# Performance work log

Hardware: AMD Instinct MI355X
Metric: run time of the kernel (lower is better)

Reference implementation:

```python
import jax, jax.numpy as jnp
import numpy as np

E = 1024
H = 16
HD = E // H


def setup_inputs() -> dict:
    key = jax.random.key(0)
    k1, k2, k3, k4, k5 = jax.random.split(key, 5)
    x = jax.random.normal(k1, (2, 2048, E), dtype=jnp.float32)
    s = 1.0 / np.sqrt(E)
    qkv_w = jax.random.uniform(k2, (3 * E, E), jnp.float32, -s, s)
    qkv_b = jax.random.uniform(k3, (3 * E,), jnp.float32, -s, s)
    o_w = jax.random.uniform(k4, (E, E), jnp.float32, -s, s)
    o_b = jax.random.uniform(k5, (E,), jnp.float32, -s, s)
    return {"x": x, "qkv_w": qkv_w, "qkv_b": qkv_b, "o_w": o_w, "o_b": o_b}


def reference(x, qkv_w, qkv_b, o_w, o_b):
    B, T, _ = x.shape
    # qkv projection (torch Linear: x @ W.T + b)
    qkv = x @ qkv_w.T + qkv_b  # [B,T,3E]
    q, k, v = jnp.split(qkv, 3, axis=-1)
    # [B,H,T,HD]
    q = q.reshape(B, T, H, HD).transpose(0, 2, 1, 3)
    k = k.reshape(B, T, H, HD).transpose(0, 2, 1, 3)
    v = v.reshape(B, T, H, HD).transpose(0, 2, 1, 3)
    scores = jnp.einsum('bhqd,bhkd->bhqk', q, k) / np.sqrt(HD)
    causal = jnp.tril(jnp.ones((T, T), dtype=bool))
    scores = jnp.where(causal, scores, -jnp.inf)
    attn = jax.nn.softmax(scores, axis=-1)  # dropout disabled (eval mode)
    y = jnp.einsum('bhqk,bhkd->bhqd', attn, v)
    y = y.transpose(0, 2, 1, 3).reshape(B, T, E)
    return y @ o_w.T + o_b
```

## Files before the change

kernel.cpp:

```cpp
#include <hip/hip_runtime.h>
#include <hip/hip_bf16.h>
#include <math.h>

#define BATCH 2
#define SEQ   2048
#define EMB   1024
#define NH    16
#define HD    64
#define M_ROWS (BATCH * SEQ)

typedef __attribute__((ext_vector_type(8))) short bf16x8;
typedef __attribute__((ext_vector_type(4))) float f32x4;

__device__ __forceinline__ ushort f2bf(float f) {
    unsigned u = __float_as_uint(f);
    unsigned lsb = (u >> 16) & 1u;
    u += 0x7fffu + lsb;
    return (ushort)(u >> 16);
}

__device__ __forceinline__ unsigned cvt_pk_bf16(float lo, float hi) {
    unsigned r;
    asm("v_cvt_pk_bf16_f32 %0, %1, %2" : "=v"(r) : "v"(lo), "v"(hi));
    return r;
}

__device__ __forceinline__ void gload_lds16(const void* g, void* l) {
    __builtin_amdgcn_global_load_lds(
        (const __attribute__((address_space(1))) unsigned int*)g,
        (__attribute__((address_space(3))) unsigned int*)l, 16, 0, 0);
}

__global__ __launch_bounds__(256) void cvt3_f32_bf16(
    const float* __restrict__ s1, const float* __restrict__ s2,
    const float* __restrict__ s3, ushort* __restrict__ out,
    int n1, int n2)
{
    int i = (blockIdx.x * 256 + threadIdx.x) * 4;
    const float* src;
    int off;
    if (i < n1)            { src = s1; off = i; }
    else if (i < n1 + n2)  { src = s2; off = i - n1; }
    else                   { src = s3; off = i - n1 - n2; }
    float4 v = *reinterpret_cast<const float4*>(&src[off]);
    uint2 pk;
    pk.x = cvt_pk_bf16(v.x, v.y);
    pk.y = cvt_pk_bf16(v.z, v.w);
    *reinterpret_cast<uint2*>(&out[i]) = pk;
}

template <int MODE>
__global__ __launch_bounds__(256) void gemm_mfma_abt(
    const ushort* __restrict__ A, const ushort* __restrict__ B,
    const float* __restrict__ bias, float* __restrict__ Cout,
    ushort* __restrict__ qkb, ushort* __restrict__ vtb,
    int M, int N, int K)
{
    __shared__ ushort Al[128 * 64];
    __shared__ ushort Bl[128 * 64];

    const int tid  = threadIdx.x;
    const int lane = tid & 63;
    const int wave = tid >> 6;
    const int wr   = wave >> 1;
    const int wc   = wave & 1;
    const int l15  = lane & 15;
    const int l4   = lane >> 4;
    const int m0   = blockIdx.y * 128;
    const int n0   = blockIdx.x * 128;

    f32x4 acc[4][4];
#pragma unroll
    for (int m = 0; m < 4; ++m)
#pragma unroll
        for (int n = 0; n < 4; ++n)
#pragma unroll
            for (int r = 0; r < 4; ++r) acc[m][n][r] = 0.f;

    for (int k0 = 0; k0 < K; k0 += 64) {
#pragma unroll
        for (int it = 0; it < 4; ++it) {
            int chunk = tid + it * 256;
            int row = chunk >> 3;
            int kc  = (chunk & 7) * 8;
            gload_lds16(&A[(size_t)(m0 + row) * K + k0 + kc], &Al[chunk * 8]);
            gload_lds16(&B[(size_t)(n0 + row) * K + k0 + kc], &Bl[chunk * 8]);
        }
        __syncthreads();

#pragma unroll
        for (int kk = 0; kk < 2; ++kk) {
            const int ko = kk * 32 + l4 * 8;
            bf16x8 a[4], b[4];
#pragma unroll
            for (int m = 0; m < 4; ++m)
                a[m] = *reinterpret_cast<const bf16x8*>(
                    &Al[(wr * 64 + m * 16 + l15) * 64 + ko]);
#pragma unroll
            for (int n = 0; n < 4; ++n)
                b[n] = *reinterpret_cast<const bf16x8*>(
                    &Bl[(wc * 64 + n * 16 + l15) * 64 + ko]);
            __builtin_amdgcn_s_setprio(1);
#pragma unroll
            for (int m = 0; m < 4; ++m)
#pragma unroll
                for (int n = 0; n < 4; ++n)
                    acc[m][n] = __builtin_amdgcn_mfma_f32_16x16x32_bf16(
                        a[m], b[n], acc[m][n], 0, 0, 0);
            __builtin_amdgcn_s_setprio(0);
        }
        __syncthreads();
    }

#pragma unroll
    for (int n = 0; n < 4; ++n) {
        const int col = n0 + wc * 64 + n * 16 + l15;
        const float bv = bias[col];
        if (MODE == 0) {
#pragma unroll
            for (int m = 0; m < 4; ++m) {
                const int row0 = m0 + wr * 64 + m * 16 + l4 * 4;
#pragma unroll
                for (int r = 0; r < 4; ++r)
                    Cout[(size_t)(row0 + r) * N + col] = acc[m][n][r] + bv;
            }
        } else if (col < 2 * EMB) {
#pragma unroll
            for (int m = 0; m < 4; ++m) {
                const int row0 = m0 + wr * 64 + m * 16 + l4 * 4;
#pragma unroll
                for (int r = 0; r < 4; ++r)
                    qkb[(size_t)(row0 + r) * 2048 + col] = f2bf(acc[m][n][r] + bv);
            }
        } else {
            const int h = (col - 2 * EMB) >> 6;
            const int d = col & 63;
#pragma unroll
            for (int m = 0; m < 4; ++m) {
                const int row0 = m0 + wr * 64 + m * 16 + l4 * 4;
                const int bb = row0 >> 11;
                const int t  = row0 & 2047;
                uint2 pk;
                pk.x = cvt_pk_bf16(acc[m][n][0] + bv, acc[m][n][1] + bv);
                pk.y = cvt_pk_bf16(acc[m][n][2] + bv, acc[m][n][3] + bv);
                *reinterpret_cast<uint2*>(
                    &vtb[((size_t)(bb * 16 + h) * 64 + d) * 2048 + t]) = pk;
            }
        }
    }
}

__global__ __launch_bounds__(512) void attn_mfma(
    const ushort* __restrict__ qk, const ushort* __restrict__ vt,
    ushort* __restrict__ y)
{
    __shared__ alignas(16) ushort Kl[4][4096];
    __shared__ alignas(16) ushort Vl[4][4096];
    __shared__ alignas(16) ushort QP[8192];

    const int tid  = threadIdx.x;
    const int lane = tid & 63;
    const int w    = tid >> 6;
    const int l15  = lane & 15;
    const int l4   = lane >> 4;

    const int id  = blockIdx.x;
    const int xcd = id & 7;
    const int bh  = xcd * 4 + ((id >> 3) & 3);
    const int pp  = id >> 5;
    const int b   = bh >> 4;
    const int h   = bh & 15;

    const ushort* qbase = qk + (size_t)b * SEQ * 2048 + h * HD;
    const ushort* kbase = qbase + EMB;
    const ushort* vbase = vt + (size_t)bh * HD * SEQ;

    const int swz   = (l15 & 7) << 4;
    const int koff0 = ((l4 * 16) ^ swz) >> 1;
    const int koff1 = ((64 + l4 * 16) ^ swz) >> 1;

    int pso[4];
#pragma unroll
    for (int n = 0; n < 4; ++n) pso[n] = ((n * 32 + l4 * 8) ^ swz) >> 1;

    const short OBF = (short)0x3F80;
    const bf16x8 ones = {OBF, OBF, OBF, OBF, OBF, OBF, OBF, OBF};
    const float BETA = 0.18033688f;

    const int qrow = (w * 16 + l15) * 64;

    const int sr = tid >> 3;
    const int sc = ((tid & 7) ^ (sr & 7)) << 3;
    const int i2 = tid + 512;
    const int qr2 = i2 >> 3;
    const int qc2 = ((i2 & 7) ^ (qr2 & 7)) << 3;

#pragma unroll
    for (int pass = 0; pass < 2; ++pass) {
        const int qt  = pass ? (15 - pp) : pp;
        const int nkv = 2 * qt + 2;

        gload_lds16(qbase + (size_t)(qt * 128 + sr) * 2048 + sc, &QP[tid * 8]);
        gload_lds16(qbase + (size_t)(qt * 128 + qr2) * 2048 + qc2, &QP[i2 * 8]);
        gload_lds16(kbase + (size_t)sr * 2048 + sc, &Kl[0][tid * 8]);
        gload_lds16(kbase + (size_t)(64 + sr) * 2048 + sc, &Kl[1][tid * 8]);
        gload_lds16(vbase + (size_t)sr * 2048 + sc, &Vl[0][tid * 8]);
        gload_lds16(vbase + (size_t)sr * 2048 + 64 + sc, &Vl[1][tid * 8]);
        __syncthreads();

        const bf16x8 qf0 = *reinterpret_cast<const bf16x8*>(&QP[qrow + koff0]);
        const bf16x8 qf1 = *reinterpret_cast<const bf16x8*>(&QP[qrow + koff1]);

        f32x4 o[4];
#pragma unroll
        for (int n = 0; n < 4; ++n)
#pragma unroll
            for (int r = 0; r < 4; ++r) o[n][r] = 0.f;
        f32x4 lacc = {0.f, 0.f, 0.f, 0.f};
        float m = -3.0e38f;

        auto computeTile = [&](const ushort* Kb, const ushort* Vb, int kkt) {
            bf16x8 kf[4][2];
#pragma unroll
            for (int n = 0; n < 4; ++n) {
                kf[n][0] = *reinterpret_cast<const bf16x8*>(
                    &Kb[(n * 16 + l15) * 64 + koff0]);
                kf[n][1] = *reinterpret_cast<const bf16x8*>(
                    &Kb[(n * 16 + l15) * 64 + koff1]);
            }
            f32x4 s[4];
            __builtin_amdgcn_s_setprio(1);
#pragma unroll
            for (int n = 0; n < 4; ++n) {
                f32x4 z = {0.f, 0.f, 0.f, 0.f};
                z = __builtin_amdgcn_mfma_f32_16x16x32_bf16(kf[n][0], qf0, z, 0, 0, 0);
                s[n] = __builtin_amdgcn_mfma_f32_16x16x32_bf16(kf[n][1], qf1, z, 0, 0, 0);
            }
            __builtin_amdgcn_s_setprio(0);

            bf16x8 vf[4][2];
#pragma unroll
            for (int n = 0; n < 4; ++n) {
                vf[n][0] = *reinterpret_cast<const bf16x8*>(
                    &Vb[(n * 16 + l15) * 64 + koff0]);
                vf[n][1] = *reinterpret_cast<const bf16x8*>(
                    &Vb[(n * 16 + l15) * 64 + koff1]);
            }

            if (kkt >= nkv - 2) {
                const int q0 = qt * 128 + w * 16 + l15;
#pragma unroll
                for (int n = 0; n < 4; ++n)
#pragma unroll
                    for (int r = 0; r < 4; ++r) {
                        int kg = kkt * 64 + n * 16 + l4 * 4 + r;
                        if (kg > q0) s[n][r] = -3.0e38f;
                    }
            }

            float a0 = fmaxf(fmaxf(s[0][0], s[0][1]), fmaxf(s[0][2], s[0][3]));
            float a1 = fmaxf(fmaxf(s[1][0], s[1][1]), fmaxf(s[1][2], s[1][3]));
            float a2 = fmaxf(fmaxf(s[2][0], s[2][1]), fmaxf(s[2][2], s[2][3]));
            float a3 = fmaxf(fmaxf(s[3][0], s[3][1]), fmaxf(s[3][2], s[3][3]));
            float pm = fmaxf(fmaxf(a0, a1), fmaxf(a2, a3)) * BETA;

            if (__any(pm > m + 8.0f)) {
                float tm = fmaxf(pm, __shfl_xor(pm, 16));
                tm = fmaxf(tm, __shfl_xor(tm, 32));
                float mn = fmaxf(m, tm);
                float al = exp2f(m - mn);
                m = mn;
                float b0 = __shfl(al, l4 * 4 + 0, 16);
                float b1 = __shfl(al, l4 * 4 + 1, 16);
                float b2 = __shfl(al, l4 * 4 + 2, 16);
                float b3 = __shfl(al, l4 * 4 + 3, 16);
                lacc[0] *= b0; lacc[1] *= b1; lacc[2] *= b2; lacc[3] *= b3;
#pragma unroll
                for (int n = 0; n < 4; ++n) {
                    o[n][0] *= b0; o[n][1] *= b1; o[n][2] *= b2; o[n][3] *= b3;
                }
            }

#pragma unroll
            for (int n = 0; n < 4; ++n) {
                float pa = exp2f(fmaf(s[n][0], BETA, -m));
                float pb = exp2f(fmaf(s[n][1], BETA, -m));
                float pc = exp2f(fmaf(s[n][2], BETA, -m));
                float pd = exp2f(fmaf(s[n][3], BETA, -m));
                uint2 pk;
                pk.x = cvt_pk_bf16(pa, pb);
                pk.y = cvt_pk_bf16(pc, pd);
                *reinterpret_cast<uint2*>(&QP[qrow + pso[n]]) = pk;
            }

            bf16x8 pf0 = *reinterpret_cast<const bf16x8*>(&QP[qrow + koff0]);
            bf16x8 pf1 = *reinterpret_cast<const bf16x8*>(&QP[qrow + koff1]);
            __builtin_amdgcn_s_setprio(1);
            lacc = __builtin_amdgcn_mfma_f32_16x16x32_bf16(pf0, ones, lacc, 0, 0, 0);
            lacc = __builtin_amdgcn_mfma_f32_16x16x32_bf16(pf1, ones, lacc, 0, 0, 0);
#pragma unroll
            for (int n = 0; n < 4; ++n) {
                o[n] = __builtin_amdgcn_mfma_f32_16x16x32_bf16(pf0, vf[n][0], o[n], 0, 0, 0);
                o[n] = __builtin_amdgcn_mfma_f32_16x16x32_bf16(pf1, vf[n][1], o[n], 0, 0, 0);
            }
            __builtin_amdgcn_s_setprio(0);
        };

        for (int kk = 0; kk < nkv; kk += 2) {
            if (kk + 2 < nkv) {
                const int b2 = (kk + 2) & 3;
                const int b3 = (kk + 3) & 3;
                gload_lds16(kbase + (size_t)((kk + 2) * 64 + sr) * 2048 + sc,
                            &Kl[b2][tid * 8]);
                gload_lds16(kbase + (size_t)((kk + 3) * 64 + sr) * 2048 + sc,
                            &Kl[b3][tid * 8]);
                gload_lds16(vbase + (size_t)sr * 2048 + (kk + 2) * 64 + sc,
                            &Vl[b2][tid * 8]);
                gload_lds16(vbase + (size_t)sr * 2048 + (kk + 3) * 64 + sc,
                            &Vl[b3][tid * 8]);
            }
            computeTile(Kl[kk & 3], Vl[kk & 3], kk);
            computeTile(Kl[(kk + 1) & 3], Vl[(kk + 1) & 3], kk + 1);
            __syncthreads();
        }

#pragma unroll
        for (int r = 0; r < 4; ++r) {
            float inv = 1.f / lacc[r];
            int row = qt * 128 + w * 16 + l4 * 4 + r;
#pragma unroll
            for (int n = 0; n < 4; ++n) {
                y[(size_t)(b * SEQ + row) * EMB + h * HD + n * 16 + l15] =
                    f2bf(o[n][r] * inv);
            }
        }
        __syncthreads();
    }
}

extern "C" void kernel_launch(void* const* d_in, const int* in_sizes, int n_in,
                              void* d_out, int out_size, void* d_ws, size_t ws_size,
                              hipStream_t stream)
{
    const float* x     = (const float*)d_in[0];
    const float* qkv_w = (const float*)d_in[1];
    const float* qkv_b = (const float*)d_in[2];
    const float* o_w   = (const float*)d_in[3];
    const float* o_b   = (const float*)d_in[4];
    float* out = (float*)d_out;

    ushort* xb    = (ushort*)d_ws;
    ushort* wqkvb = xb    + (size_t)M_ROWS * EMB;
    ushort* owb   = wqkvb + (size_t)3 * EMB * EMB;
    ushort* qkb   = owb   + (size_t)EMB * EMB;
    ushort* vtb   = qkb   + (size_t)M_ROWS * 2 * EMB;
    ushort* ybb   = vtb   + (size_t)32 * HD * SEQ;

    {
        int n1 = M_ROWS * EMB;
        int n2 = 3 * EMB * EMB;
        int ntot = n1 + n2 + EMB * EMB;
        cvt3_f32_bf16<<<ntot / 1024, 256, 0, stream>>>(
            x, qkv_w, o_w, xb, n1, n2);
    }

    {
        dim3 grid(3 * EMB / 128, M_ROWS / 128);
        gemm_mfma_abt<1><<<grid, 256, 0, stream>>>(
            xb, wqkvb, qkv_b, nullptr, qkb, vtb, M_ROWS, 3 * EMB, EMB);
    }

    {
        attn_mfma<<<256, 512, 0, stream>>>(qkb, vtb, ybb);
    }

    {
        dim3 grid(EMB / 128, M_ROWS / 128);
        gemm_mfma_abt<0><<<grid, 256, 0, stream>>>(
            ybb, owb, o_b, out, nullptr, nullptr, M_ROWS, EMB, EMB);
    }
}
```

Before: 113.7 us.

## Split attention KV loop across two wave groups with split-K merge for balanced work

The attention block grows from 512 to 1024 threads. Instead of running the two paired query tiles one after the other, group B handles the first 17 KV tiles of the long query tile. Group A handles its short tile and then the remaining KV tiles of the long tile. The partial softmax states (o, l, m) are merged through LDS at the end. This cuts the serial KV loop per block from 34 tiles to 17 and raises occupancy, at the cost of double-buffered KV loads, an extra LDS merge and more register pressure at the higher launch bound.

```diff
diff --git a/kernel.cpp b/kernel.cpp
--- a/kernel.cpp
+++ b/kernel.cpp
@@ -150,17 +150,18 @@
     }
 }
 
-__global__ __launch_bounds__(512) void attn_mfma(
+__global__ __launch_bounds__(1024) void attn_mfma(
     const ushort* __restrict__ qk, const ushort* __restrict__ vt,
     ushort* __restrict__ y)
 {
-    __shared__ alignas(16) ushort Kl[4][4096];
-    __shared__ alignas(16) ushort Vl[4][4096];
-    __shared__ alignas(16) ushort QP[8192];
+    __shared__ alignas(16) ushort KV[8][4096];
+    __shared__ alignas(16) ushort QP[16384];
 
     const int tid  = threadIdx.x;
     const int lane = tid & 63;
     const int w    = tid >> 6;
+    const int u    = w & 7;
+    const bool isA = (w < 8);
     const int l15  = lane & 15;
     const int l4   = lane >> 4;
 
@@ -168,6 +169,9 @@
     const int xcd = id & 7;
     const int bh  = xcd * 4 + ((id >> 3) & 3);
     const int pp  = id >> 5;
+    const int qtA = pp, qtB = 15 - pp;
+    const int nkvA = 2 * pp + 2;
+    const int nkvB = 32 - 2 * pp;
     const int b   = bh >> 4;
     const int h   = bh & 15;
 
@@ -178,7 +182,6 @@
     const int swz   = (l15 & 7) << 4;
     const int koff0 = ((l4 * 16) ^ swz) >> 1;
     const int koff1 = ((64 + l4 * 16) ^ swz) >> 1;
-
     int pso[4];
 #pragma unroll
     for (int n = 0; n < 4; ++n) pso[n] = ((n * 32 + l4 * 8) ^ swz) >> 1;
@@ -189,152 +192,214 @@
 
     const int qrow = (w * 16 + l15) * 64;
 
-    const int sr = tid >> 3;
-    const int sc = ((tid & 7) ^ (sr & 7)) << 3;
-    const int i2 = tid + 512;
-    const int qr2 = i2 >> 3;
-    const int qc2 = ((i2 & 7) ^ (qr2 & 7)) << 3;
-
-#pragma unroll
-    for (int pass = 0; pass < 2; ++pass) {
-        const int qt  = pass ? (15 - pp) : pp;
-        const int nkv = 2 * qt + 2;
-
-        gload_lds16(qbase + (size_t)(qt * 128 + sr) * 2048 + sc, &QP[tid * 8]);
-        gload_lds16(qbase + (size_t)(qt * 128 + qr2) * 2048 + qc2, &QP[i2 * 8]);
-        gload_lds16(kbase + (size_t)sr * 2048 + sc, &Kl[0][tid * 8]);
-        gload_lds16(kbase + (size_t)(64 + sr) * 2048 + sc, &Kl[1][tid * 8]);
-        gload_lds16(vbase + (size_t)sr * 2048 + sc, &Vl[0][tid * 8]);
-        gload_lds16(vbase + (size_t)sr * 2048 + 64 + sc, &Vl[1][tid * 8]);
-        __syncthreads();
-
-        const bf16x8 qf0 = *reinterpret_cast<const bf16x8*>(&QP[qrow + koff0]);
-        const bf16x8 qf1 = *reinterpret_cast<const bf16x8*>(&QP[qrow + koff1]);
-
-        f32x4 o[4];
-#pragma unroll
-        for (int n = 0; n < 4; ++n)
-#pragma unroll
-            for (int r = 0; r < 4; ++r) o[n][r] = 0.f;
-        f32x4 lacc = {0.f, 0.f, 0.f, 0.f};
-        float m = -3.0e38f;
-
-        auto computeTile = [&](const ushort* Kb, const ushort* Vb, int kkt) {
-            bf16x8 kf[4][2];
-#pragma unroll
-            for (int n = 0; n < 4; ++n) {
-                kf[n][0] = *reinterpret_cast<const bf16x8*>(
-                    &Kb[(n * 16 + l15) * 64 + koff0]);
-                kf[n][1] = *reinterpret_cast<const bf16x8*>(
-                    &Kb[(n * 16 + l15) * 64 + koff1]);
-            }
-            f32x4 s[4];
-            __builtin_amdgcn_s_setprio(1);
-#pragma unroll
-            for (int n = 0; n < 4; ++n) {
-                f32x4 z = {0.f, 0.f, 0.f, 0.f};
-                z = __builtin_amdgcn_mfma_f32_16x16x32_bf16(kf[n][0], qf0, z, 0, 0, 0);
-                s[n] = __builtin_amdgcn_mfma_f32_16x16x32_bf16(kf[n][1], qf1, z, 0, 0, 0);
-            }
-            __builtin_amdgcn_s_setprio(0);
-
-            bf16x8 vf[4][2];
-#pragma unroll
-            for (int n = 0; n < 4; ++n) {
-                vf[n][0] = *reinterpret_cast<const bf16x8*>(
-                    &Vb[(n * 16 + l15) * 64 + koff0]);
-                vf[n][1] = *reinterpret_cast<const bf16x8*>(
-                    &Vb[(n * 16 + l15) * 64 + koff1]);
-            }
-
-            if (kkt >= nkv - 2) {
-                const int q0 = qt * 128 + w * 16 + l15;
-#pragma unroll
-                for (int n = 0; n < 4; ++n)
-#pragma unroll
-                    for (int r = 0; r < 4; ++r) {
-                        int kg = kkt * 64 + n * 16 + l4 * 4 + r;
-                        if (kg > q0) s[n][r] = -3.0e38f;
-                    }
-            }
-
-            float a0 = fmaxf(fmaxf(s[0][0], s[0][1]), fmaxf(s[0][2], s[0][3]));
-            float a1 = fmaxf(fmaxf(s[1][0], s[1][1]), fmaxf(s[1][2], s[1][3]));
-            float a2 = fmaxf(fmaxf(s[2][0], s[2][1]), fmaxf(s[2][2], s[2][3]));
-            float a3 = fmaxf(fmaxf(s[3][0], s[3][1]), fmaxf(s[3][2], s[3][3]));
-            float pm = fmaxf(fmaxf(a0, a1), fmaxf(a2, a3)) * BETA;
-
-            if (__any(pm > m + 8.0f)) {
-                float tm = fmaxf(pm, __shfl_xor(pm, 16));
-                tm = fmaxf(tm, __shfl_xor(tm, 32));
-                float mn = fmaxf(m, tm);
-                float al = exp2f(m - mn);
-                m = mn;
-                float b0 = __shfl(al, l4 * 4 + 0, 16);
-                float b1 = __shfl(al, l4 * 4 + 1, 16);
-                float b2 = __shfl(al, l4 * 4 + 2, 16);
-                float b3 = __shfl(al, l4 * 4 + 3, 16);
-                lacc[0] *= b0; lacc[1] *= b1; lacc[2] *= b2; lacc[3] *= b3;
-#pragma unroll
-                for (int n = 0; n < 4; ++n) {
-                    o[n][0] *= b0; o[n][1] *= b1; o[n][2] *= b2; o[n][3] *= b3;
-                }
-            }
-
-#pragma unroll
-            for (int n = 0; n < 4; ++n) {
-                float pa = exp2f(fmaf(s[n][0], BETA, -m));
-                float pb = exp2f(fmaf(s[n][1], BETA, -m));
-                float pc = exp2f(fmaf(s[n][2], BETA, -m));
-                float pd = exp2f(fmaf(s[n][3], BETA, -m));
-                uint2 pk;
-                pk.x = cvt_pk_bf16(pa, pb);
-                pk.y = cvt_pk_bf16(pc, pd);
-                *reinterpret_cast<uint2*>(&QP[qrow + pso[n]]) = pk;
-            }
-
-            bf16x8 pf0 = *reinterpret_cast<const bf16x8*>(&QP[qrow + koff0]);
-            bf16x8 pf1 = *reinterpret_cast<const bf16x8*>(&QP[qrow + koff1]);
-            __builtin_amdgcn_s_setprio(1);
-            lacc = __builtin_amdgcn_mfma_f32_16x16x32_bf16(pf0, ones, lacc, 0, 0, 0);
-            lacc = __builtin_amdgcn_mfma_f32_16x16x32_bf16(pf1, ones, lacc, 0, 0, 0);
-#pragma unroll
-            for (int n = 0; n < 4; ++n) {
-                o[n] = __builtin_amdgcn_mfma_f32_16x16x32_bf16(pf0, vf[n][0], o[n], 0, 0, 0);
-                o[n] = __builtin_amdgcn_mfma_f32_16x16x32_bf16(pf1, vf[n][1], o[n], 0, 0, 0);
-            }
-            __builtin_amdgcn_s_setprio(0);
-        };
-
-        for (int kk = 0; kk < nkv; kk += 2) {
-            if (kk + 2 < nkv) {
-                const int b2 = (kk + 2) & 3;
-                const int b3 = (kk + 3) & 3;
-                gload_lds16(kbase + (size_t)((kk + 2) * 64 + sr) * 2048 + sc,
-                            &Kl[b2][tid * 8]);
-                gload_lds16(kbase + (size_t)((kk + 3) * 64 + sr) * 2048 + sc,
-                            &Kl[b3][tid * 8]);
-                gload_lds16(vbase + (size_t)sr * 2048 + (kk + 2) * 64 + sc,
-                            &Vl[b2][tid * 8]);
-                gload_lds16(vbase + (size_t)sr * 2048 + (kk + 3) * 64 + sc,
-                            &Vl[b3][tid * 8]);
-            }
-            computeTile(Kl[kk & 3], Vl[kk & 3], kk);
-            computeTile(Kl[(kk + 1) & 3], Vl[(kk + 1) & 3], kk + 1);
-            __syncthreads();
-        }
-
+    const int st = tid & 511;
+    const int fr = st >> 3;
+    const int fc = ((st & 7) ^ (fr & 7)) << 3;
+
+#pragma unroll
+    for (int it = 0; it < 2; ++it) {
+        int c = tid + it * 1024;
+        int qs = c >> 10;
+        int r  = (c >> 3) & 127;
+        int cc = ((c & 7) ^ (r & 7)) << 3;
+        int grow = (qs ? qtB : qtA) * 128 + r;
+        gload_lds16(qbase + (size_t)grow * 2048 + cc, &QP[c * 8]);
+    }
+    if (tid < 512) {
+        gload_lds16(kbase + (size_t)fr * 2048 + fc, &KV[0][st * 8]);
+        gload_lds16(vbase + (size_t)fr * 2048 + fc, &KV[4][st * 8]);
+    }
+    __syncthreads();
+
+    bf16x8 qfA0, qfA1, qfB0, qfB1;
+    if (isA) {
+        qfA0 = *reinterpret_cast<const bf16x8*>(&QP[(u * 16 + l15) * 64 + koff0]);
+        qfA1 = *reinterpret_cast<const bf16x8*>(&QP[(u * 16 + l15) * 64 + koff1]);
+    }
+    qfB0 = *reinterpret_cast<const bf16x8*>(&QP[(128 + u * 16 + l15) * 64 + koff0]);
+    qfB1 = *reinterpret_cast<const bf16x8*>(&QP[(128 + u * 16 + l15) * 64 + koff1]);
+    __syncthreads();
+
+    f32x4 o[4];
+    f32x4 lacc;
+    float m;
+#pragma unroll
+    for (int n = 0; n < 4; ++n)
+#pragma unroll
+        for (int r = 0; r < 4; ++r) o[n][r] = 0.f;
+    lacc[0] = lacc[1] = lacc[2] = lacc[3] = 0.f;
+    m = -3.0e38f;
+
+    auto writeOut = [&](int qtile) {
 #pragma unroll
         for (int r = 0; r < 4; ++r) {
             float inv = 1.f / lacc[r];
-            int row = qt * 128 + w * 16 + l4 * 4 + r;
+            int row = qtile * 128 + u * 16 + l4 * 4 + r;
 #pragma unroll
             for (int n = 0; n < 4; ++n) {
                 y[(size_t)(b * SEQ + row) * EMB + h * HD + n * 16 + l15] =
                     f2bf(o[n][r] * inv);
             }
         }
+    };
+
+    auto computeTile = [&](const ushort* Kb, const ushort* Vb, int tile,
+                           int nkvL, int q0, const bf16x8& qf0, const bf16x8& qf1) {
+        bf16x8 kf[4][2];
+#pragma unroll
+        for (int n = 0; n < 4; ++n) {
+            kf[n][0] = *reinterpret_cast<const bf16x8*>(
+                &Kb[(n * 16 + l15) * 64 + koff0]);
+            kf[n][1] = *reinterpret_cast<const bf16x8*>(
+                &Kb[(n * 16 + l15) * 64 + koff1]);
+        }
+        f32x4 s[4];
+        __builtin_amdgcn_s_setprio(1);
+#pragma unroll
+        for (int n = 0; n < 4; ++n) {
+            f32x4 z = {0.f, 0.f, 0.f, 0.f};
+            z = __builtin_amdgcn_mfma_f32_16x16x32_bf16(kf[n][0], qf0, z, 0, 0, 0);
+            s[n] = __builtin_amdgcn_mfma_f32_16x16x32_bf16(kf[n][1], qf1, z, 0, 0, 0);
+        }
+        __builtin_amdgcn_s_setprio(0);
+
+        bf16x8 vf[4][2];
+#pragma unroll
+        for (int n = 0; n < 4; ++n) {
+            vf[n][0] = *reinterpret_cast<const bf16x8*>(
+                &Vb[(n * 16 + l15) * 64 + koff0]);
+            vf[n][1] = *reinterpret_cast<const bf16x8*>(
+                &Vb[(n * 16 + l15) * 64 + koff1]);
+        }
+
+        if (tile >= nkvL - 2) {
+#pragma unroll
+            for (int n = 0; n < 4; ++n)
+#pragma unroll
+                for (int r = 0; r < 4; ++r) {
+                    int kg = tile * 64 + n * 16 + l4 * 4 + r;
+                    if (kg > q0) s[n][r] = -3.0e38f;
+                }
+        }
+
+        float a0 = fmaxf(fmaxf(s[0][0], s[0][1]), fmaxf(s[0][2], s[0][3]));
+        float a1 = fmaxf(fmaxf(s[1][0], s[1][1]), fmaxf(s[1][2], s[1][3]));
+        float a2 = fmaxf(fmaxf(s[2][0], s[2][1]), fmaxf(s[2][2], s[2][3]));
+        float a3 = fmaxf(fmaxf(s[3][0], s[3][1]), fmaxf(s[3][2], s[3][3]));
+        float pm = fmaxf(fmaxf(a0, a1), fmaxf(a2, a3)) * BETA;
+
+        if (__any(pm > m + 8.0f)) {
+            float tm = fmaxf(pm, __shfl_xor(pm, 16));
+            tm = fmaxf(tm, __shfl_xor(tm, 32));
+            float mn = fmaxf(m, tm);
+            float al = exp2f(m - mn);
+            m = mn;
+            float b0 = __shfl(al, l4 * 4 + 0, 16);
+            float b1 = __shfl(al, l4 * 4 + 1, 16);
+            float b2 = __shfl(al, l4 * 4 + 2, 16);
+            float b3 = __shfl(al, l4 * 4 + 3, 16);
+            lacc[0] *= b0; lacc[1] *= b1; lacc[2] *= b2; lacc[3] *= b3;
+#pragma unroll
+            for (int n = 0; n < 4; ++n) {
+                o[n][0] *= b0; o[n][1] *= b1; o[n][2] *= b2; o[n][3] *= b3;
+            }
+        }
+
+#pragma unroll
+        for (int n = 0; n < 4; ++n) {
+            float pa = exp2f(fmaf(s[n][0], BETA, -m));
+            float pb = exp2f(fmaf(s[n][1], BETA, -m));
+            float pc = exp2f(fmaf(s[n][2], BETA, -m));
+            float pd = exp2f(fmaf(s[n][3], BETA, -m));
+            uint2 pk;
+            pk.x = cvt_pk_bf16(pa, pb);
+            pk.y = cvt_pk_bf16(pc, pd);
+            *reinterpret_cast<uint2*>(&QP[qrow + pso[n]]) = pk;
+        }
+
+        bf16x8 pf0 = *reinterpret_cast<const bf16x8*>(&QP[qrow + koff0]);
+        bf16x8 pf1 = *reinterpret_cast<const bf16x8*>(&QP[qrow + koff1]);
+        __builtin_amdgcn_s_setprio(1);
+        lacc = __builtin_amdgcn_mfma_f32_16x16x32_bf16(pf0, ones, lacc, 0, 0, 0);
+        lacc = __builtin_amdgcn_mfma_f32_16x16x32_bf16(pf1, ones, lacc, 0, 0, 0);
+#pragma unroll
+        for (int n = 0; n < 4; ++n) {
+            o[n] = __builtin_amdgcn_mfma_f32_16x16x32_bf16(pf0, vf[n][0], o[n], 0, 0, 0);
+            o[n] = __builtin_amdgcn_mfma_f32_16x16x32_bf16(pf1, vf[n][1], o[n], 0, 0, 0);
+        }
+        __builtin_amdgcn_s_setprio(0);
+    };
+
+    for (int i = 0; i < 17; ++i) {
+        if (i < 16) {
+            int nf = i + 1;
+            if (tid < 512) {
+                gload_lds16(kbase + (size_t)(nf * 64 + fr) * 2048 + fc,
+                            &KV[nf & 1][st * 8]);
+                gload_lds16(vbase + (size_t)fr * 2048 + nf * 64 + fc,
+                            &KV[4 + (nf & 1)][st * 8]);
+            } else if (nf >= nkvA) {
+                int tt = 17 + (nf - nkvA);
+                gload_lds16(kbase + (size_t)(tt * 64 + fr) * 2048 + fc,
+                            &KV[2 + (tt & 1)][st * 8]);
+                gload_lds16(vbase + (size_t)fr * 2048 + tt * 64 + fc,
+                            &KV[6 + (tt & 1)][st * 8]);
+            }
+        }
+
+        if (isA) {
+            if (i == nkvA) {
+                writeOut(qtA);
+#pragma unroll
+                for (int n = 0; n < 4; ++n)
+#pragma unroll
+                    for (int r = 0; r < 4; ++r) o[n][r] = 0.f;
+                lacc[0] = lacc[1] = lacc[2] = lacc[3] = 0.f;
+                m = -3.0e38f;
+            }
+            if (i < nkvA) {
+                computeTile(KV[i & 1], KV[4 + (i & 1)], i, nkvA,
+                            qtA * 128 + u * 16 + l15, qfA0, qfA1);
+            } else {
+                int tt = 17 + (i - nkvA);
+                computeTile(KV[2 + (tt & 1)], KV[6 + (tt & 1)], tt, nkvB,
+                            qtB * 128 + u * 16 + l15, qfB0, qfB1);
+            }
+        } else {
+            computeTile(KV[i & 1], KV[4 + (i & 1)], i, nkvB,
+                        qtB * 128 + u * 16 + l15, qfB0, qfB1);
+        }
         __syncthreads();
+    }
+
+    float* mbuf = reinterpret_cast<float*>(&KV[0][0]);
+    if (isA) {
+        int base = (u * 64 + lane) * 21;
+#pragma unroll
+        for (int n = 0; n < 4; ++n)
+#pragma unroll
+            for (int r = 0; r < 4; ++r) mbuf[base + n * 4 + r] = o[n][r];
+#pragma unroll
+        for (int r = 0; r < 4; ++r) mbuf[base + 16 + r] = lacc[r];
+        mbuf[base + 20] = m;
+    }
+    __syncthreads();
+    if (!isA) {
+        int base = (u * 64 + lane) * 21;
+        float mt = mbuf[base + 20];
+        float M  = fmaxf(m, mt);
+        float fh = exp2f(m - M);
+        float ft = exp2f(mt - M);
+#pragma unroll
+        for (int r = 0; r < 4; ++r) {
+            float fhr = __shfl(fh, l4 * 4 + r, 16);
+            float ftr = __shfl(ft, l4 * 4 + r, 16);
+            lacc[r] = lacc[r] * fhr + mbuf[base + 16 + r] * ftr;
+#pragma unroll
+            for (int n = 0; n < 4; ++n)
+                o[n][r] = o[n][r] * fhr + mbuf[base + n * 4 + r] * ftr;
+        }
+        writeOut(qtB);
     }
 }
 
@@ -371,7 +436,7 @@
     }
 
     {
-        attn_mfma<<<256, 512, 0, stream>>>(qkb, vtb, ybb);
+        attn_mfma<<<256, 1024, 0, stream>>>(qkb, vtb, ybb);
     }
 
     {
```

Measured after the change: 120.4 us. +5.9%, slower.

## Deepen attention K/V prefetch to four tiles and fold softmax scale into Q

Applied to the files above, without the earlier changes.

The attention kernel's K/V staging grows from 4 to 8 LDS buffers, so it prefetches four 64-key tiles ahead and runs four tiles per barrier instead of two. This is meant to hide more global-load latency and cut synchronisation count. Separately, the QKV projection epilogue now multiplies Q by the softmax scale (including log2e) before writing bf16, which removes the per-score multiply in the softmax. In exchange, LDS use rises to about 144KB per block, which likely drops residency to one block per CU. Q is also rounded to bf16 after scaling, which shifts rounding slightly.

```diff
diff --git a/kernel.cpp b/kernel.cpp
--- a/kernel.cpp
+++ b/kernel.cpp
@@ -125,12 +125,14 @@
                     Cout[(size_t)(row0 + r) * N + col] = acc[m][n][r] + bv;
             }
         } else if (col < 2 * EMB) {
+            const float qs = (col < EMB) ? 0.18033688f : 1.0f;
 #pragma unroll
             for (int m = 0; m < 4; ++m) {
                 const int row0 = m0 + wr * 64 + m * 16 + l4 * 4;
 #pragma unroll
                 for (int r = 0; r < 4; ++r)
-                    qkb[(size_t)(row0 + r) * 2048 + col] = f2bf(acc[m][n][r] + bv);
+                    qkb[(size_t)(row0 + r) * 2048 + col] =
+                        f2bf((acc[m][n][r] + bv) * qs);
             }
         } else {
             const int h = (col - 2 * EMB) >> 6;
@@ -154,8 +156,8 @@
     const ushort* __restrict__ qk, const ushort* __restrict__ vt,
     ushort* __restrict__ y)
 {
-    __shared__ alignas(16) ushort Kl[4][4096];
-    __shared__ alignas(16) ushort Vl[4][4096];
+    __shared__ alignas(16) ushort Kl[8][4096];
+    __shared__ alignas(16) ushort Vl[8][4096];
     __shared__ alignas(16) ushort QP[8192];
 
     const int tid  = threadIdx.x;
@@ -185,7 +187,6 @@
 
     const short OBF = (short)0x3F80;
     const bf16x8 ones = {OBF, OBF, OBF, OBF, OBF, OBF, OBF, OBF};
-    const float BETA = 0.18033688f;
 
     const int qrow = (w * 16 + l15) * 64;
 
@@ -202,10 +203,11 @@
 
         gload_lds16(qbase + (size_t)(qt * 128 + sr) * 2048 + sc, &QP[tid * 8]);
         gload_lds16(qbase + (size_t)(qt * 128 + qr2) * 2048 + qc2, &QP[i2 * 8]);
-        gload_lds16(kbase + (size_t)sr * 2048 + sc, &Kl[0][tid * 8]);
-        gload_lds16(kbase + (size_t)(64 + sr) * 2048 + sc, &Kl[1][tid * 8]);
-        gload_lds16(vbase + (size_t)sr * 2048 + sc, &Vl[0][tid * 8]);
-        gload_lds16(vbase + (size_t)sr * 2048 + 64 + sc, &Vl[1][tid * 8]);
+#pragma unroll
+        for (int t = 0; t < 4; ++t) {
+            gload_lds16(kbase + (size_t)(t * 64 + sr) * 2048 + sc, &Kl[t][tid * 8]);
+            gload_lds16(vbase + (size_t)sr * 2048 + t * 64 + sc, &Vl[t][tid * 8]);
+        }
         __syncthreads();
 
         const bf16x8 qf0 = *reinterpret_cast<const bf16x8*>(&QP[qrow + koff0]);
@@ -262,7 +264,7 @@
             float a1 = fmaxf(fmaxf(s[1][0], s[1][1]), fmaxf(s[1][2], s[1][3]));
             float a2 = fmaxf(fmaxf(s[2][0], s[2][1]), fmaxf(s[2][2], s[2][3]));
             float a3 = fmaxf(fmaxf(s[3][0], s[3][1]), fmaxf(s[3][2], s[3][3]));
-            float pm = fmaxf(fmaxf(a0, a1), fmaxf(a2, a3)) * BETA;
+            float pm = fmaxf(fmaxf(a0, a1), fmaxf(a2, a3));
 
             if (__any(pm > m + 8.0f)) {
                 float tm = fmaxf(pm, __shfl_xor(pm, 16));
@@ -283,10 +285,10 @@
 
 #pragma unroll
             for (int n = 0; n < 4; ++n) {
-                float pa = exp2f(fmaf(s[n][0], BETA, -m));
-                float pb = exp2f(fmaf(s[n][1], BETA, -m));
-                float pc = exp2f(fmaf(s[n][2], BETA, -m));
-                float pd = exp2f(fmaf(s[n][3], BETA, -m));
+                float pa = exp2f(s[n][0] - m);
+                float pb = exp2f(s[n][1] - m);
+                float pc = exp2f(s[n][2] - m);
+                float pd = exp2f(s[n][3] - m);
                 uint2 pk;
                 pk.x = cvt_pk_bf16(pa, pb);
                 pk.y = cvt_pk_bf16(pc, pd);
@@ -306,21 +308,22 @@
             __builtin_amdgcn_s_setprio(0);
         };
 
-        for (int kk = 0; kk < nkv; kk += 2) {
-            if (kk + 2 < nkv) {
-                const int b2 = (kk + 2) & 3;
-                const int b3 = (kk + 3) & 3;
-                gload_lds16(kbase + (size_t)((kk + 2) * 64 + sr) * 2048 + sc,
-                            &Kl[b2][tid * 8]);
-                gload_lds16(kbase + (size_t)((kk + 3) * 64 + sr) * 2048 + sc,
-                            &Kl[b3][tid * 8]);
-                gload_lds16(vbase + (size_t)sr * 2048 + (kk + 2) * 64 + sc,
-                            &Vl[b2][tid * 8]);
-                gload_lds16(vbase + (size_t)sr * 2048 + (kk + 3) * 64 + sc,
-                            &Vl[b3][tid * 8]);
-            }
-            computeTile(Kl[kk & 3], Vl[kk & 3], kk);
-            computeTile(Kl[(kk + 1) & 3], Vl[(kk + 1) & 3], kk + 1);
+        for (int kk = 0; kk < nkv; kk += 4) {
+#pragma unroll
+            for (int j = 0; j < 4; ++j) {
+                int t = kk + 4 + j;
+                if (t < nkv) {
+                    gload_lds16(kbase + (size_t)(t * 64 + sr) * 2048 + sc,
+                                &Kl[t & 7][tid * 8]);
+                    gload_lds16(vbase + (size_t)sr * 2048 + t * 64 + sc,
+                                &Vl[t & 7][tid * 8]);
+                }
+            }
+#pragma unroll
+            for (int j = 0; j < 4; ++j) {
+                int t = kk + j;
+                if (t < nkv) computeTile(Kl[t & 7], Vl[t & 7], t);
+            }
             __syncthreads();
         }
 
```

Result: no change. 114.8 us (+1.0%).

## Batch QK^T MFMAs for two KV tiles and fold softmax scale into Q

Applied to the files above, without the earlier changes.

Q is now pre-scaled by the softmax constant (including log2e) in the QKV projection epilogue, so the attention loop drops the per-element multiply in the max and exp paths. The attention loop issues all K fragment loads and QK^T MFMAs for both 64-key tiles of an iteration before running softmax and PV for each tile. This gives the MFMA pipe more independent work to overlap with LDS loads and the exp math. The P staging buffer is doubled so each tile has its own region, which raises LDS use and register pressure, and Q is rounded to bf16 after scaling.

```diff
diff --git a/kernel.cpp b/kernel.cpp
--- a/kernel.cpp
+++ b/kernel.cpp
@@ -125,12 +125,14 @@
                     Cout[(size_t)(row0 + r) * N + col] = acc[m][n][r] + bv;
             }
         } else if (col < 2 * EMB) {
+            const float qs = (col < EMB) ? 0.18033688f : 1.0f;
 #pragma unroll
             for (int m = 0; m < 4; ++m) {
                 const int row0 = m0 + wr * 64 + m * 16 + l4 * 4;
 #pragma unroll
                 for (int r = 0; r < 4; ++r)
-                    qkb[(size_t)(row0 + r) * 2048 + col] = f2bf(acc[m][n][r] + bv);
+                    qkb[(size_t)(row0 + r) * 2048 + col] =
+                        f2bf((acc[m][n][r] + bv) * qs);
             }
         } else {
             const int h = (col - 2 * EMB) >> 6;
@@ -156,7 +158,7 @@
 {
     __shared__ alignas(16) ushort Kl[4][4096];
     __shared__ alignas(16) ushort Vl[4][4096];
-    __shared__ alignas(16) ushort QP[8192];
+    __shared__ alignas(16) ushort QP[16384];
 
     const int tid  = threadIdx.x;
     const int lane = tid & 63;
@@ -185,9 +187,9 @@
 
     const short OBF = (short)0x3F80;
     const bf16x8 ones = {OBF, OBF, OBF, OBF, OBF, OBF, OBF, OBF};
-    const float BETA = 0.18033688f;
-
-    const int qrow = (w * 16 + l15) * 64;
+
+    const int qrowA = (w * 16 + l15) * 64;
+    const int qrowB = qrowA + 128 * 64;
 
     const int sr = tid >> 3;
     const int sc = ((tid & 7) ^ (sr & 7)) << 3;
@@ -208,8 +210,8 @@
         gload_lds16(vbase + (size_t)sr * 2048 + 64 + sc, &Vl[1][tid * 8]);
         __syncthreads();
 
-        const bf16x8 qf0 = *reinterpret_cast<const bf16x8*>(&QP[qrow + koff0]);
-        const bf16x8 qf1 = *reinterpret_cast<const bf16x8*>(&QP[qrow + koff1]);
+        const bf16x8 qf0 = *reinterpret_cast<const bf16x8*>(&QP[qrowA + koff0]);
+        const bf16x8 qf1 = *reinterpret_cast<const bf16x8*>(&QP[qrowA + koff1]);
 
         f32x4 o[4];
 #pragma unroll
@@ -219,50 +221,14 @@
         f32x4 lacc = {0.f, 0.f, 0.f, 0.f};
         float m = -3.0e38f;
 
-        auto computeTile = [&](const ushort* Kb, const ushort* Vb, int kkt) {
-            bf16x8 kf[4][2];
-#pragma unroll
-            for (int n = 0; n < 4; ++n) {
-                kf[n][0] = *reinterpret_cast<const bf16x8*>(
-                    &Kb[(n * 16 + l15) * 64 + koff0]);
-                kf[n][1] = *reinterpret_cast<const bf16x8*>(
-                    &Kb[(n * 16 + l15) * 64 + koff1]);
-            }
-            f32x4 s[4];
-            __builtin_amdgcn_s_setprio(1);
-#pragma unroll
-            for (int n = 0; n < 4; ++n) {
-                f32x4 z = {0.f, 0.f, 0.f, 0.f};
-                z = __builtin_amdgcn_mfma_f32_16x16x32_bf16(kf[n][0], qf0, z, 0, 0, 0);
-                s[n] = __builtin_amdgcn_mfma_f32_16x16x32_bf16(kf[n][1], qf1, z, 0, 0, 0);
-            }
-            __builtin_amdgcn_s_setprio(0);
-
-            bf16x8 vf[4][2];
-#pragma unroll
-            for (int n = 0; n < 4; ++n) {
-                vf[n][0] = *reinterpret_cast<const bf16x8*>(
-                    &Vb[(n * 16 + l15) * 64 + koff0]);
-                vf[n][1] = *reinterpret_cast<const bf16x8*>(
-                    &Vb[(n * 16 + l15) * 64 + koff1]);
-            }
-
-            if (kkt >= nkv - 2) {
-                const int q0 = qt * 128 + w * 16 + l15;
-#pragma unroll
-                for (int n = 0; n < 4; ++n)
-#pragma unroll
-                    for (int r = 0; r < 4; ++r) {
-                        int kg = kkt * 64 + n * 16 + l4 * 4 + r;
-                        if (kg > q0) s[n][r] = -3.0e38f;
-                    }
-            }
-
+        const int q0g = qt * 128 + w * 16 + l15;
+
+        auto softmaxPV = [&](f32x4 (&s)[4], const bf16x8 vf[4][2], int prow) {
             float a0 = fmaxf(fmaxf(s[0][0], s[0][1]), fmaxf(s[0][2], s[0][3]));
             float a1 = fmaxf(fmaxf(s[1][0], s[1][1]), fmaxf(s[1][2], s[1][3]));
             float a2 = fmaxf(fmaxf(s[2][0], s[2][1]), fmaxf(s[2][2], s[2][3]));
             float a3 = fmaxf(fmaxf(s[3][0], s[3][1]), fmaxf(s[3][2], s[3][3]));
-            float pm = fmaxf(fmaxf(a0, a1), fmaxf(a2, a3)) * BETA;
+            float pm = fmaxf(fmaxf(a0, a1), fmaxf(a2, a3));
 
             if (__any(pm > m + 8.0f)) {
                 float tm = fmaxf(pm, __shfl_xor(pm, 16));
@@ -283,18 +249,18 @@
 
 #pragma unroll
             for (int n = 0; n < 4; ++n) {
-                float pa = exp2f(fmaf(s[n][0], BETA, -m));
-                float pb = exp2f(fmaf(s[n][1], BETA, -m));
-                float pc = exp2f(fmaf(s[n][2], BETA, -m));
-                float pd = exp2f(fmaf(s[n][3], BETA, -m));
+                float pa = exp2f(s[n][0] - m);
+                float pb = exp2f(s[n][1] - m);
+                float pc = exp2f(s[n][2] - m);
+                float pd = exp2f(s[n][3] - m);
                 uint2 pk;
                 pk.x = cvt_pk_bf16(pa, pb);
                 pk.y = cvt_pk_bf16(pc, pd);
-                *reinterpret_cast<uint2*>(&QP[qrow + pso[n]]) = pk;
-            }
-
-            bf16x8 pf0 = *reinterpret_cast<const bf16x8*>(&QP[qrow + koff0]);
-            bf16x8 pf1 = *reinterpret_cast<const bf16x8*>(&QP[qrow + koff1]);
+                *reinterpret_cast<uint2*>(&QP[prow + pso[n]]) = pk;
+            }
+
+            bf16x8 pf0 = *reinterpret_cast<const bf16x8*>(&QP[prow + koff0]);
+            bf16x8 pf1 = *reinterpret_cast<const bf16x8*>(&QP[prow + koff1]);
             __builtin_amdgcn_s_setprio(1);
             lacc = __builtin_amdgcn_mfma_f32_16x16x32_bf16(pf0, ones, lacc, 0, 0, 0);
             lacc = __builtin_amdgcn_mfma_f32_16x16x32_bf16(pf1, ones, lacc, 0, 0, 0);
@@ -319,8 +285,63 @@
                 gload_lds16(vbase + (size_t)sr * 2048 + (kk + 3) * 64 + sc,
                             &Vl[b3][tid * 8]);
             }
-            computeTile(Kl[kk & 3], Vl[kk & 3], kk);
-            computeTile(Kl[(kk + 1) & 3], Vl[(kk + 1) & 3], kk + 1);
+
+            const ushort* KbA = Kl[kk & 3];
+            const ushort* KbB = Kl[(kk + 1) & 3];
+            const ushort* VbA = Vl[kk & 3];
+            const ushort* VbB = Vl[(kk + 1) & 3];
+
+            bf16x8 kfA[4][2], kfB[4][2];
+#pragma unroll
+            for (int n = 0; n < 4; ++n) {
+                kfA[n][0] = *reinterpret_cast<const bf16x8*>(
+                    &KbA[(n * 16 + l15) * 64 + koff0]);
+                kfA[n][1] = *reinterpret_cast<const bf16x8*>(
+                    &KbA[(n * 16 + l15) * 64 + koff1]);
+                kfB[n][0] = *reinterpret_cast<const bf16x8*>(
+                    &KbB[(n * 16 + l15) * 64 + koff0]);
+                kfB[n][1] = *reinterpret_cast<const bf16x8*>(
+                    &KbB[(n * 16 + l15) * 64 + koff1]);
+            }
+            f32x4 sA[4], sB[4];
+            __builtin_amdgcn_s_setprio(1);
+#pragma unroll
+            for (int n = 0; n < 4; ++n) {
+                f32x4 zA = {0.f, 0.f, 0.f, 0.f};
+                zA = __builtin_amdgcn_mfma_f32_16x16x32_bf16(kfA[n][0], qf0, zA, 0, 0, 0);
+                sA[n] = __builtin_amdgcn_mfma_f32_16x16x32_bf16(kfA[n][1], qf1, zA, 0, 0, 0);
+                f32x4 zB = {0.f, 0.f, 0.f, 0.f};
+                zB = __builtin_amdgcn_mfma_f32_16x16x32_bf16(kfB[n][0], qf0, zB, 0, 0, 0);
+                sB[n] = __builtin_amdgcn_mfma_f32_16x16x32_bf16(kfB[n][1], qf1, zB, 0, 0, 0);
+            }
+            __builtin_amdgcn_s_setprio(0);
+
+            bf16x8 vfA[4][2], vfB[4][2];
+#pragma unroll
+            for (int n = 0; n < 4; ++n) {
+                vfA[n][0] = *reinterpret_cast<const bf16x8*>(
+                    &VbA[(n * 16 + l15) * 64 + koff0]);
+                vfA[n][1] = *reinterpret_cast<const bf16x8*>(
+                    &VbA[(n * 16 + l15) * 64 + koff1]);
+                vfB[n][0] = *reinterpret_cast<const bf16x8*>(
+                    &VbB[(n * 16 + l15) * 64 + koff0]);
+                vfB[n][1] = *reinterpret_cast<const bf16x8*>(
+                    &VbB[(n * 16 + l15) * 64 + koff1]);
+            }
+
+            if (kk >= nkv - 2) {
+#pragma unroll
+                for (int n = 0; n < 4; ++n)
+#pragma unroll
+                    for (int r = 0; r < 4; ++r) {
+                        int kgA = kk * 64 + n * 16 + l4 * 4 + r;
+                        if (kgA > q0g)      sA[n][r] = -3.0e38f;
+                        if (kgA + 64 > q0g) sB[n][r] = -3.0e38f;
+                    }
+            }
+
+            softmaxPV(sA, vfA, qrowA);
+            softmaxPV(sB, vfB, qrowB);
             __syncthreads();
         }
 
```

New measurement: 113.8 us. Within noise of the previous version (+0.1%).
